# Performance work log

Hardware: AMD Instinct MI355X
Metric: run time of the kernel (lower is better)

Reference implementation:

```python
import jax, jax.numpy as jnp
import numpy as np
from jax import lax

N = 1024          # n_ligand == n_receptor == feature dim (required by broadcast in source)
D = 1024          # gnn_input_dim == gnn_output_dim
H = 32            # hopi_output_dim
C = 32            # cnn_channels


def setup_inputs() -> dict:
    key = jax.random.key(0)
    ks = jax.random.split(key, 24)
    s = 0.02
    inp = {
        "ligand_node_features": jax.random.normal(ks[0], (N, D), jnp.float32),
        "ligand_edge_features": jax.random.normal(ks[1], (N, D), jnp.float32),
        "ligand_adjacency": jax.random.uniform(ks[2], (N, N), jnp.float32),
        "receptor_node_features": jax.random.normal(ks[3], (N, D), jnp.float32),
        "receptor_edge_features": jax.random.normal(ks[4], (N, D), jnp.float32),
        "receptor_adjacency": jax.random.uniform(ks[5], (N, N), jnp.float32),
        # GNNLayer params (shared between ligand and receptor, as in source)
        "Wn": jax.random.normal(ks[6], (D, D), jnp.float32) * s,
        "bn": jax.random.normal(ks[7], (D,), jnp.float32) * s,
        "We": jax.random.normal(ks[8], (D, D), jnp.float32) * s,
        "be": jax.random.normal(ks[9], (D,), jnp.float32) * s,
        "Wa": jax.random.normal(ks[10], (1, D), jnp.float32) * s,
        "ba": jax.random.normal(ks[11], (1,), jnp.float32) * s,
        # HighOrderPairwiseInteraction: Linear(2*D -> H)
        "W_hopi": jax.random.normal(ks[12], (H, 2 * D), jnp.float32) * s,
        "b_hopi": jax.random.normal(ks[13], (H,), jnp.float32) * s,
        # CNN tail
        "conv1_w": jax.random.normal(ks[14], (C, H, 3, 3), jnp.float32) * s,
        "conv1_b": jax.random.normal(ks[15], (C,), jnp.float32) * s,
        "conv2_w": jax.random.normal(ks[16], (C, C, 3, 3), jnp.float32) * s,
        "conv2_b": jax.random.normal(ks[17], (C,), jnp.float32) * s,
        "conv3_w": jax.random.normal(ks[18], (1, C, 1, 1), jnp.float32) * s,
        "conv3_b": jax.random.normal(ks[19], (1,), jnp.float32) * s,
    }
    return inp


def _gnn(nf, ef, Wn, bn, We, be, Wa, ba):
    # aggregated: [N, D]
    agg = jnp.tanh(nf @ Wn.T + bn + ef @ We.T + be)
    scores = agg @ Wa.T + ba                      # [N, 1]
    attn = jax.nn.softmax(scores, axis=1)         # softmax over size-1 dim -> ones (faithful)
    weighted = jnp.sum(agg * attn, axis=1)        # [N]
    return nf + weighted                          # [N,D] + [N] broadcasts over last dim (D == N)


def _conv(x, w, b):
    y = lax.conv_general_dilated(x, w, (1, 1), "SAME",
                                 dimension_numbers=("NCHW", "OIHW", "NCHW"))
    return y + b[None, :, None, None]


def reference(ligand_node_features, ligand_edge_features, ligand_adjacency,
              receptor_node_features, receptor_edge_features, receptor_adjacency,
              Wn, bn, We, be, Wa, ba, W_hopi, b_hopi,
              conv1_w, conv1_b, conv2_w, conv2_b, conv3_w, conv3_b):
    lig = _gnn(ligand_node_features, ligand_edge_features, Wn, bn, We, be, Wa, ba)
    rec = _gnn(receptor_node_features, receptor_edge_features, Wn, bn, We, be, Wa, ba)

    # HOPI: interactions[i, j] = Linear(cat(lig[i], rec[j])) == lig[i] @ Wl.T + rec[j] @ Wr.T + b
    Wl, Wr = W_hopi[:, :D], W_hopi[:, D:]
    lig_p = lig @ Wl.T                            # [N, H]
    rec_p = rec @ Wr.T                            # [N, H]
    interactions = lig_p[:, None, :] + rec_p[None, :, :] + b_hopi  # [N, N, H]

    x = jnp.transpose(interactions, (2, 0, 1))[None]  # [1, H, N, N]
    x = jax.nn.relu(_conv(x, conv1_w, conv1_b))
    x = jax.nn.relu(_conv(x, conv2_w, conv2_b))
    x = _conv(x, conv3_w, conv3_b)                # [1, 1, N, N]
    return x[0, 0]                                # [N, N]
```

## Files before the change

### kernel.cpp

```cpp
#include <hip/hip_runtime.h>


typedef _Float16 half8 __attribute__((ext_vector_type(8)));
typedef _Float16 half4 __attribute__((ext_vector_type(4)));
typedef float    f32x4 __attribute__((ext_vector_type(4)));

__device__ __forceinline__ short f2h_bits(float f){
    _Float16 h = (_Float16)f;
    return __builtin_bit_cast(short, h);
}
__device__ __forceinline__ half8 pack2(const float4& x, const float4& y){
    half8 r;
    r[0] = (_Float16)x.x; r[1] = (_Float16)x.y;
    r[2] = (_Float16)x.z; r[3] = (_Float16)x.w;
    r[4] = (_Float16)y.x; r[5] = (_Float16)y.y;
    r[6] = (_Float16)y.z; r[7] = (_Float16)y.w;
    return r;
}
__device__ __forceinline__ half4 pack4(const float4& x){
    half4 r;
    r[0] = (_Float16)x.x; r[1] = (_Float16)x.y;
    r[2] = (_Float16)x.z; r[3] = (_Float16)x.w;
    return r;
}
__device__ __forceinline__ float tanh_fast(float x){
    float e = __expf(2.f * x);
    return 1.f - 2.f / (e + 1.f);
}

#define SWZ(c) ((((c) >> 1) & 3) << 3)

#define GNN_LOAD(AV, BV, KBN) {                                              \
    const int kbn_ = (KBN) & 2047;                                           \
    const float* Asrc_ = (kbn_ < 1024) ? A0 : A1;                            \
    const float* Bsrc_ = (kbn_ < 1024) ? Wn : We;                            \
    const int kk_ = kbn_ & 1023;                                             \
    const float* ap_ = Asrc_ + (size_t)(j0 + arow) * 1024 + kk_ + akc;       \
    const float* bp_ = Bsrc_ + (size_t)(d0 + brow) * 1024 + kk_ + bkc;       \
    AV[0] = *reinterpret_cast<const float4*>(ap_);                           \
    AV[1] = *reinterpret_cast<const float4*>(ap_ + 4);                       \
    AV[2] = *reinterpret_cast<const float4*>(ap_ + 8);                       \
    AV[3] = *reinterpret_cast<const float4*>(ap_ + 12);                      \
    BV[0] = *reinterpret_cast<const float4*>(bp_);                           \
    BV[1] = *reinterpret_cast<const float4*>(bp_ + 4);                       \
}

#define GNN_STAGE(AV, BV) {                                                  \
    const int ga_ = (t & 3) * 2;                                             \
    const int sa_ = arow & 7;                                                \
    *reinterpret_cast<half8*>(&As[arow * 64 + ((ga_    ) ^ sa_) * 8]) = pack2(AV[0], AV[1]); \
    *reinterpret_cast<half8*>(&As[arow * 64 + ((ga_ + 1) ^ sa_) * 8]) = pack2(AV[2], AV[3]); \
    *reinterpret_cast<half8*>(&Bs[brow * 64 + ((t & 7) ^ (brow & 7)) * 8]) = pack2(BV[0], BV[1]); \
}

#define GNN_MFMA() {                                                         \
    _Pragma("unroll")                                                        \
    for (int ks = 0; ks < 2; ++ks){                                          \
        half8 Af[2], Bf[2];                                                  \
        _Pragma("unroll")                                                    \
        for (int m = 0; m < 2; ++m){                                         \
            int row = wm * 32 + m * 16 + lr;                                 \
            int g   = ((ks * 4 + lg) ^ (row & 7)) * 8;                       \
            Af[m] = *reinterpret_cast<const half8*>(&As[row * 64 + g]);      \
        }                                                                    \
        _Pragma("unroll")                                                    \
        for (int n = 0; n < 2; ++n){                                         \
            int col = wn * 32 + n * 16 + lr;                                 \
            int g   = ((ks * 4 + lg) ^ (col & 7)) * 8;                       \
            Bf[n] = *reinterpret_cast<const half8*>(&Bs[col * 64 + g]);      \
        }                                                                    \
        _Pragma("unroll")                                                    \
        for (int m = 0; m < 2; ++m)                                          \
            _Pragma("unroll")                                                \
            for (int n = 0; n < 2; ++n)                                      \
                acc[m][n] = __builtin_amdgcn_mfma_f32_16x16x32_f16(          \
                    Af[m], Bf[n], acc[m][n], 0, 0, 0);                       \
    }                                                                        \
}

__global__ __launch_bounds__(512) void gnn_kernel(
    const float* __restrict__ lig_nf, const float* __restrict__ lig_ef,
    const float* __restrict__ rec_nf, const float* __restrict__ rec_ef,
    const float* __restrict__ Wn, const float* __restrict__ We,
    const float* __restrict__ bn, const float* __restrict__ be,
    float* __restrict__ part)
{
    __shared__ __attribute__((aligned(16))) short As[128 * 64];
    __shared__ __attribute__((aligned(16))) short Bs[64 * 64];
    __shared__ float red[128][2];

    const int t  = threadIdx.x;
    const int cx = blockIdx.z;
    const float* A0 = cx ? rec_nf : lig_nf;
    const float* A1 = cx ? rec_ef : lig_ef;
    const int j0 = blockIdx.x * 128;
    const int d0 = blockIdx.y * 64;

    const int wid  = t >> 6;
    const int wm   = wid >> 1;
    const int wn   = wid & 1;
    const int lane = t & 63;
    const int lr   = lane & 15;
    const int lg   = lane >> 4;

    f32x4 acc[2][2];
    #pragma unroll
    for (int m = 0; m < 2; ++m)
        #pragma unroll
        for (int n = 0; n < 2; ++n)
            acc[m][n] = (f32x4){0.f, 0.f, 0.f, 0.f};

    const int arow = t >> 2;
    const int akc  = (t & 3) * 16;
    const int brow = t >> 3;
    const int bkc  = (t & 7) * 8;

    float4 avA[4], bvA[2], avB[4], bvB[2];
    GNN_LOAD(avA, bvA, 0);
    GNN_LOAD(avB, bvB, 64);

    for (int kb = 0; kb < 2048; kb += 128){
        __syncthreads();
        GNN_STAGE(avA, bvA);
        GNN_LOAD(avA, bvA, kb + 128);
        __syncthreads();
        GNN_MFMA();
        __syncthreads();
        GNN_STAGE(avB, bvB);
        GNN_LOAD(avB, bvB, kb + 192);
        __syncthreads();
        GNN_MFMA();
    }

    float rowsum[2][4];
    #pragma unroll
    for (int m = 0; m < 2; ++m)
        #pragma unroll
        for (int jj = 0; jj < 4; ++jj) rowsum[m][jj] = 0.f;
    #pragma unroll
    for (int n = 0; n < 2; ++n){
        int d = d0 + wn * 32 + n * 16 + lr;
        float bias = bn[d] + be[d];
        #pragma unroll
        for (int m = 0; m < 2; ++m)
            #pragma unroll
            for (int jj = 0; jj < 4; ++jj)
                rowsum[m][jj] += tanh_fast(acc[m][n][jj] + bias);
    }
    #pragma unroll
    for (int mask = 1; mask < 16; mask <<= 1)
        #pragma unroll
        for (int m = 0; m < 2; ++m)
            #pragma unroll
            for (int jj = 0; jj < 4; ++jj)
                rowsum[m][jj] += __shfl_xor(rowsum[m][jj], mask);
    __syncthreads();
    if (lr == 0){
        #pragma unroll
        for (int m = 0; m < 2; ++m)
            #pragma unroll
            for (int jj = 0; jj < 4; ++jj)
                red[wm * 32 + m * 16 + lg * 4 + jj][wn] = rowsum[m][jj];
    }
    __syncthreads();
    if (t < 128)
        part[(size_t)cx * 16384 + (size_t)blockIdx.y * 1024 + j0 + t]
            = red[t][0] + red[t][1];
}

#define PP_LOAD(AV, BV, KBN) {                                               \
    const int kcol_ = (KBN) & 1023;                                          \
    _Pragma("unroll")                                                        \
    for (int p = 0; p < 3; ++p){                                             \
        int e_ = t + 512 * p;                                                \
        if (e_ < 1280){                                                      \
            int rowl_ = e_ >> 4;                                             \
            int grow_ = r0 - 8 + rowl_;                                      \
            if ((unsigned)grow_ < 1024u)                                     \
                AV[p] = *reinterpret_cast<const float4*>(                    \
                    nf + (size_t)grow_ * 1024 + kcol_ + (e_ & 15) * 4);      \
            else                                                             \
                AV[p] = make_float4(0.f, 0.f, 0.f, 0.f);                     \
        }                                                                    \
    }                                                                        \
    BV = *reinterpret_cast<const float4*>(                                   \
        W + (size_t)(t >> 4) * 2048 + kcol_ + (t & 15) * 4);                 \
}

#define PP_STAGE(AV, BV) {                                                   \
    _Pragma("unroll")                                                        \
    for (int p = 0; p < 3; ++p){                                             \
        int e_ = t + 512 * p;                                                \
        if (e_ < 1280){                                                      \
            int rowl_ = e_ >> 4;                                             \
            int ga_ = (e_ & 15) >> 1;                                        \
            int sub_ = (e_ & 1) * 4;                                         \
            *reinterpret_cast<half4*>(                                       \
                &As[rowl_ * 64 + ((ga_ ^ (rowl_ & 7)) * 8) + sub_]) = pack4(AV[p]); \
        }                                                                    \
    }                                                                        \
    {                                                                        \
        int row_ = t >> 4;                                                   \
        int ga_ = (t & 15) >> 1;                                             \
        int sub_ = (t & 1) * 4;                                              \
        *reinterpret_cast<half4*>(                                           \
            &Bs[row_ * 64 + ((ga_ ^ (row_ & 7)) * 8) + sub_]) = pack4(BV);   \
    }                                                                        \
}

#define PP_MFMA() {                                                          \
    if (wid < 5){                                                            \
        _Pragma("unroll")                                                    \
        for (int ks = 0; ks < 2; ++ks){                                      \
            int ar_ = wid * 16 + lr;                                         \
            half8 Af = *reinterpret_cast<const half8*>(                      \
                &As[ar_ * 64 + ((ks * 4 + lg) ^ (ar_ & 7)) * 8]);            \
            _Pragma("unroll")                                                \
            for (int n = 0; n < 2; ++n){                                     \
                int col_ = n * 16 + lr;                                      \
                half8 Bf = *reinterpret_cast<const half8*>(                  \
                    &Bs[col_ * 64 + ((ks * 4 + lg) ^ (col_ & 7)) * 8]);      \
                pacc[n] = __builtin_amdgcn_mfma_f32_16x16x32_f16(            \
                    Af, Bf, pacc[n], 0, 0, 0);                               \
            }                                                                \
        }                                                                    \
    }                                                                        \
}

__global__ __launch_bounds__(512) void pp_kernel(
    const float* __restrict__ lig_nf, const float* __restrict__ rec_nf,
    const float* __restrict__ W_hopi, const float* __restrict__ b_hopi,
    const float* __restrict__ w1, const float* __restrict__ b1,
    const float* __restrict__ w2,
    const float* __restrict__ part,
    float* __restrict__ Kp, short* __restrict__ U16, short* __restrict__ V16,
    short* __restrict__ w2f16)
{
    __shared__ __attribute__((aligned(16))) char smem[47232];
    const int t = threadIdx.x;
    const int role = blockIdx.x;

    if (role < 32){
        short* As = reinterpret_cast<short*>(smem);
        short* Bs = reinterpret_cast<short*>(smem + 10240);
        short* Pz = reinterpret_cast<short*>(smem + 14336);
        short* Ws = reinterpret_cast<short*>(smem + 20736);

        const int cx = role >> 4;
        const int r0 = (role & 15) * 64;
        const float* nf = cx ? rec_nf : lig_nf;
        const float* W  = W_hopi + (cx ? 1024 : 0);
        short* O = cx ? V16 : U16;

        const int wid = t >> 6;
        const int lane = t & 63;
        const int lr = lane & 15;
        const int lg = lane >> 4;

        f32x4 pacc[2];
        pacc[0] = (f32x4){0.f, 0.f, 0.f, 0.f};
        pacc[1] = (f32x4){0.f, 0.f, 0.f, 0.f};

        float4 avA[3], avB[3];
        float4 bvA, bvB;
        PP_LOAD(avA, bvA, 0);
        PP_LOAD(avB, bvB, 64);

        for (int kb = 0; kb < 1024; kb += 128){
            __syncthreads();
            PP_STAGE(avA, bvA);
            PP_LOAD(avA, bvA, kb + 128);
            __syncthreads();
            PP_MFMA();
            __syncthreads();
            PP_STAGE(avB, bvB);
            PP_LOAD(avB, bvB, kb + 192);
            __syncthreads();
            PP_MFMA();
        }

        if (wid < 5){
            #pragma unroll
            for (int n = 0; n < 2; ++n)
                #pragma unroll
                for (int jj = 0; jj < 4; ++jj){
                    int rowl = wid * 16 + lg * 4 + jj;
                    Pz[rowl * 40 + n * 16 + lr] = f2h_bits(pacc[n][jj]);
                }
        }

        #pragma unroll
        for (int q = 0; q < 2; ++q){
            int pr = t * 2 + q;
            int co = pr >> 5;
            int ci = pr & 31;
            const float* wp = w1 + co * 288 + ci * 9;
            float tap[9];
            #pragma unroll
            for (int e = 0; e < 9; ++e) tap[e] = wp[e];
            #pragma unroll
            for (int d = 0; d < 3; ++d){
                float ta, tb, tc;
                if (cx == 0){ ta = tap[d * 3 + 0]; tb = tap[d * 3 + 1]; tc = tap[d * 3 + 2]; }
                else        { ta = tap[0 + d];     tb = tap[3 + d];     tc = tap[6 + d]; }
                Ws[(0 * 32 + co) * 104 + d * 32 + ci] = f2h_bits(ta + tb + tc);
                Ws[(1 * 32 + co) * 104 + d * 32 + ci] = f2h_bits(tb + tc);
                Ws[(2 * 32 + co) * 104 + d * 32 + ci] = f2h_bits(ta + tb);
            }
        }
        __syncthreads();

        if (wid < 4){
            f32x4 uacc[3][2];
            #pragma unroll
            for (int cs = 0; cs < 3; ++cs)
                #pragma unroll
                for (int n = 0; n < 2; ++n)
                    uacc[cs][n] = (f32x4){0.f, 0.f, 0.f, 0.f};
            #pragma unroll
            for (int d = 0; d < 3; ++d){
                int ar = wid * 16 + lr;
                half8 Ap = *reinterpret_cast<const half8*>(
                    &Pz[(7 + ar + d) * 40 + lg * 8]);
                #pragma unroll
                for (int cs = 0; cs < 3; ++cs)
                    #pragma unroll
                    for (int n = 0; n < 2; ++n){
                        half8 Bp = *reinterpret_cast<const half8*>(
                            &Ws[(cs * 32 + n * 16 + lr) * 104 + d * 32 + lg * 8]);
                        uacc[cs][n] = __builtin_amdgcn_mfma_f32_16x16x32_f16(
                            Ap, Bp, uacc[cs][n], 0, 0, 0);
                    }
            }
            #pragma unroll
            for (int cs = 0; cs < 3; ++cs)
                #pragma unroll
                for (int n = 0; n < 2; ++n)
                    #pragma unroll
                    for (int jj = 0; jj < 4; ++jj){
                        int grow = r0 + wid * 16 + lg * 4 + jj;
                        O[((size_t)(cs << 10) + grow) * 32 + n * 16 + lr]
                            = f2h_bits(uacc[cs][n][jj]);
                    }
        }
        return;
    }

    if (role == 33){
        #pragma unroll
        for (int q = 0; q < 18; ++q){
            int e = t + q * 512;
            int co  = e / 288;
            int rem = e - co * 288;
            int ci  = rem / 9;
            int tap = rem - ci * 9;
            w2f16[(tap * 32 + co) * 32 + (ci ^ SWZ(co))] = f2h_bits(w2[e]);
        }
        return;
    }

    float* ws_l = reinterpret_cast<float*>(smem);
    float* ws_r = reinterpret_cast<float*>(smem + 4096);
    float* red  = reinterpret_cast<float*>(smem + 8192);
    float* cvs  = reinterpret_cast<float*>(smem + 10240);
    float* w1s  = reinterpret_cast<float*>(smem + 10368);

    #pragma unroll
    for (int q = 0; q < 5; ++q){
        int i4 = t + q * 512;
        if (i4 < 2304)
            *reinterpret_cast<float4*>(&w1s[i4 * 4]) =
                *reinterpret_cast<const float4*>(w1 + i4 * 4);
    }
    for (int j = t; j < 1024; j += 512){
        float sl = 0.f, sr = 0.f;
        #pragma unroll
        for (int b = 0; b < 16; ++b){
            sl += part[b * 1024 + j];
            sr += part[16384 + b * 1024 + j];
        }
        ws_l[j] = sl; ws_r[j] = sr;
    }
    __syncthreads();
    {
        const int h = t & 31;
        const int seg = t >> 5;
        const float* wl = W_hopi + (size_t)h * 2048 + seg * 64;
        const float* wr = wl + 1024;
        float s = 0.f;
        #pragma unroll 8
        for (int j = 0; j < 64; j += 4){
            float4 a = *reinterpret_cast<const float4*>(wl + j);
            float4 b = *reinterpret_cast<const float4*>(wr + j);
            const float* l = &ws_l[seg * 64 + j];
            const float* r = &ws_r[seg * 64 + j];
            s = fmaf(l[0], a.x, s); s = fmaf(l[1], a.y, s);
            s = fmaf(l[2], a.z, s); s = fmaf(l[3], a.w, s);
            s = fmaf(r[0], b.x, s); s = fmaf(r[1], b.y, s);
            s = fmaf(r[2], b.z, s); s = fmaf(r[3], b.w, s);
        }
        red[t] = s;
    }
    __syncthreads();
    if (t < 32){
        float tot = b_hopi[t];
        #pragma unroll
        for (int g = 0; g < 16; ++g) tot += red[g * 32 + t];
        cvs[t] = tot;
    }
    __syncthreads();
    for (int e = t; e < 288; e += 512){
        int co  = e & 31;
        int cse = e >> 5;
        int yc  = cse / 3, xc = cse - yc * 3;
        float sum = b1[co];
        for (int ci = 0; ci < 32; ++ci){
            const float* wp = &w1s[co * 288 + ci * 9];
            float t00 = wp[0], t01 = wp[1], t02 = wp[2];
            float t10 = wp[3], t11 = wp[4], t12 = wp[5];
            float t20 = wp[6], t21 = wp[7], t22 = wp[8];
            float r0, r1, r2;
            if (xc == 0){ r0 = t00+t01+t02; r1 = t10+t11+t12; r2 = t20+t21+t22; }
            else if (xc == 1){ r0 = t01+t02; r1 = t11+t12; r2 = t21+t22; }
            else { r0 = t00+t01; r1 = t10+t11; r2 = t20+t21; }
            float wsum = (yc == 0) ? (r0+r1+r2) : ((yc == 1) ? (r1+r2) : (r0+r1));
            sum = fmaf(cvs[ci], wsum, sum);
        }
        Kp[cse * 32 + co] = sum;
    }
}

__global__ __launch_bounds__(512) void conv_kernel(
    const short* __restrict__ U16, const short* __restrict__ V16,
    const float* __restrict__ Kp, const short* __restrict__ w2f16,
    const float* __restrict__ b2,
    const float* __restrict__ w3, const float* __restrict__ b3,
    float* __restrict__ outp)
{
    __shared__ __attribute__((aligned(16))) short ys[18 * 18 * 32];
    __shared__ __attribute__((aligned(16))) short wB[9 * 32 * 32];

    const int t    = threadIdx.x;
    const int oy0  = blockIdx.y * 16;
    const int ox0  = blockIdx.x * 16;
    const int wid  = t >> 6;
    const int lane = t & 63;
    const int lr   = lane & 15;
    const int lg   = lane >> 4;

    {
        const uint4* src = reinterpret_cast<const uint4*>(w2f16);
        uint4* dst = reinterpret_cast<uint4*>(wB);
        #pragma unroll
        for (int e = t; e < 1152; e += 512)
            dst[e] = src[e];
    }
    const bool interior = (blockIdx.x >= 1) & (blockIdx.x <= 62) &
                          (blockIdx.y >= 1) & (blockIdx.y <= 62);
    if (interior){
        const int cp = (t & 7) * 4;
        half4 k00;
        {
            float4 kf = *reinterpret_cast<const float4*>(&Kp[cp]);
            k00[0] = (_Float16)kf.x; k00[1] = (_Float16)kf.y;
            k00[2] = (_Float16)kf.z; k00[3] = (_Float16)kf.w;
        }
        #pragma unroll
        for (int pass = 0; pass < 6; ++pass){
            int idx = t + pass * 512;
            if (idx < 2592){
                int po  = idx >> 3;
                int ryo = po / 18;
                int rxo = po - ryo * 18;
                int gy = oy0 - 1 + ryo, gx = ox0 - 1 + rxo;
                half4 u = *reinterpret_cast<const half4*>(&U16[gy * 32 + cp]);
                half4 v = *reinterpret_cast<const half4*>(&V16[gx * 32 + cp]);
                half4 r = u + v + k00;
                #pragma unroll
                for (int e = 0; e < 4; ++e)
                    r[e] = r[e] > (_Float16)0.f ? r[e] : (_Float16)0.f;
                *reinterpret_cast<half4*>(&ys[po * 32 + (cp ^ SWZ(rxo))]) = r;
            }
        }
    } else {
        #pragma unroll
        for (int pass = 0; pass < 6; ++pass){
            int idx = t + pass * 512;
            if (idx < 2592){
                int po  = idx >> 3;
                int cp  = (idx & 7) * 4;
                int ryo = po / 18;
                int rxo = po - ryo * 18;
                int gy = oy0 - 1 + ryo, gx = ox0 - 1 + rxo;
                half4 h = {(_Float16)0.f, (_Float16)0.f, (_Float16)0.f, (_Float16)0.f};
                if ((unsigned)gy < 1024u && (unsigned)gx < 1024u){
                    int yc = (gy == 0) ? 1 : ((gy == 1023) ? 2 : 0);
                    int xc = (gx == 0) ? 1 : ((gx == 1023) ? 2 : 0);
                    half4 u = *reinterpret_cast<const half4*>(
                        &U16[((size_t)(xc << 10) + gy) * 32 + cp]);
                    half4 v = *reinterpret_cast<const half4*>(
                        &V16[((size_t)(yc << 10) + gx) * 32 + cp]);
                    float4 k = *reinterpret_cast<const float4*>(&Kp[(yc * 3 + xc) * 32 + cp]);
                    h[0] = (_Float16)fmaxf((float)u[0] + (float)v[0] + k.x, 0.f);
                    h[1] = (_Float16)fmaxf((float)u[1] + (float)v[1] + k.y, 0.f);
                    h[2] = (_Float16)fmaxf((float)u[2] + (float)v[2] + k.z, 0.f);
                    h[3] = (_Float16)fmaxf((float)u[3] + (float)v[3] + k.w, 0.f);
                }
                *reinterpret_cast<half4*>(&ys[po * 32 + (cp ^ SWZ(rxo))]) = h;
            }
        }
    }
    __syncthreads();

    {
        half8 Bf[2][9];
        float bias[2], w3v[2];
        #pragma unroll
        for (int n = 0; n < 2; ++n){
            int co = n * 16 + lr;
            bias[n] = b2[co];
            w3v[n]  = w3[co];
            #pragma unroll
            for (int tap = 0; tap < 9; ++tap)
                Bf[n][tap] = *reinterpret_cast<const half8*>(
                    &wB[(tap * 32 + co) * 32 + ((lg * 8) ^ SWZ(co))]);
        }
        const float b3v = b3[0];
        for (int s = wid; s < 16; s += 8){
            int p  = s * 16 + lr;
            int ry = p >> 4;
            int rx = p & 15;
            f32x4 acc0 = {0.f, 0.f, 0.f, 0.f};
            f32x4 acc1 = {0.f, 0.f, 0.f, 0.f};
            #pragma unroll
            for (int tap = 0; tap < 9; ++tap){
                const int dy = tap / 3, dx = tap - (tap / 3) * 3;
                int pix = (ry + dy) * 18 + rx + dx;
                half8 A = *reinterpret_cast<const half8*>(
                    &ys[pix * 32 + ((lg * 8) ^ SWZ(rx + dx))]);
                acc0 = __builtin_amdgcn_mfma_f32_16x16x32_f16(A, Bf[0][tap], acc0, 0, 0, 0);
                acc1 = __builtin_amdgcn_mfma_f32_16x16x32_f16(A, Bf[1][tap], acc1, 0, 0, 0);
            }
            float part[4];
            #pragma unroll
            for (int j = 0; j < 4; ++j)
                part[j] = w3v[0] * fmaxf(acc0[j] + bias[0], 0.f)
                        + w3v[1] * fmaxf(acc1[j] + bias[1], 0.f);
            #pragma unroll
            for (int m = 1; m < 16; m <<= 1)
                #pragma unroll
                for (int j = 0; j < 4; ++j)
                    part[j] += __shfl_xor(part[j], m);
            if (lr == 0){
                float4 o = make_float4(part[0] + b3v, part[1] + b3v,
                                       part[2] + b3v, part[3] + b3v);
                *reinterpret_cast<float4*>(outp + (size_t)(oy0 + s) * 1024 + ox0 + lg * 4) = o;
            }
        }
    }
}

extern "C" void kernel_launch(void* const* d_in, const int* in_sizes, int n_in,
                              void* d_out, int out_size, void* d_ws, size_t ws_size,
                              hipStream_t stream)
{
    const float* lig_nf = (const float*)d_in[0];
    const float* lig_ef = (const float*)d_in[1];
    const float* rec_nf = (const float*)d_in[3];
    const float* rec_ef = (const float*)d_in[4];
    const float* Wn     = (const float*)d_in[6];
    const float* bn     = (const float*)d_in[7];
    const float* We     = (const float*)d_in[8];
    const float* be     = (const float*)d_in[9];
    const float* W_hopi = (const float*)d_in[12];
    const float* b_hopi = (const float*)d_in[13];
    const float* w1     = (const float*)d_in[14];
    const float* b1     = (const float*)d_in[15];
    const float* w2     = (const float*)d_in[16];
    const float* b2     = (const float*)d_in[17];
    const float* w3     = (const float*)d_in[18];
    const float* b3     = (const float*)d_in[19];
    float* outp = (float*)d_out;

    float* part  = (float*)d_ws;
    float* Kp    = (float*)((char*)d_ws + 393216);
    short* U16   = (short*)((char*)d_ws + 394368);
    short* V16   = (short*)((char*)d_ws + 590976);
    short* w2f16 = (short*)((char*)d_ws + 787584);

    dim3 g1(8, 16, 2);
    gnn_kernel<<<g1, 512, 0, stream>>>(lig_nf, lig_ef, rec_nf, rec_ef,
                                       Wn, We, bn, be, part);
    pp_kernel<<<34, 512, 0, stream>>>(lig_nf, rec_nf, W_hopi, b_hopi,
                                      w1, b1, w2, part, Kp, U16, V16, w2f16);
    dim3 g3(64, 64);
    conv_kernel<<<g3, 512, 0, stream>>>(U16, V16, Kp, w2f16, b2, w3, b3, outp);
}
```

Baseline: 114.0 us.

## Build conv2 A-fragments in registers instead of staging relu tile in LDS

Removes the 18x18x32 shared-memory staging of the conv1 output (relu(U+V+K)) and instead has each lane compute its MFMA A operand directly from U16/V16 rows held in registers, reusing three U and three V vectors across the nine taps. This drops the shared-memory write, the barrier and the swizzled LDS reads, and lowers LDS use, which may raise occupancy. In exchange each halo value is recomputed per tap (extra VALU adds and relus), and the border path issues more global loads per tap.

```diff
diff --git a/kernel.cpp b/kernel.cpp
--- a/kernel.cpp
+++ b/kernel.cpp
@@ -437,7 +437,6 @@
     const float* __restrict__ w3, const float* __restrict__ b3,
     float* __restrict__ outp)
 {
-    __shared__ __attribute__((aligned(16))) short ys[18 * 18 * 32];
     __shared__ __attribute__((aligned(16))) short wB[9 * 32 * 32];
 
     const int t    = threadIdx.x;
@@ -447,6 +446,7 @@
     const int lane = t & 63;
     const int lr   = lane & 15;
     const int lg   = lane >> 4;
+    const int c8   = lg * 8;
 
     {
         const uint4* src = reinterpret_cast<const uint4*>(w2f16);
@@ -455,107 +455,97 @@
         for (int e = t; e < 1152; e += 512)
             dst[e] = src[e];
     }
+    __syncthreads();
+
+    half8 Bf[2][9];
+    float bias[2], w3v[2];
+    #pragma unroll
+    for (int n = 0; n < 2; ++n){
+        int co = n * 16 + lr;
+        bias[n] = b2[co];
+        w3v[n]  = w3[co];
+        #pragma unroll
+        for (int tap = 0; tap < 9; ++tap)
+            Bf[n][tap] = *reinterpret_cast<const half8*>(
+                &wB[(tap * 32 + co) * 32 + ((lg * 8) ^ SWZ(co))]);
+    }
+    const float b3v = b3[0];
+
     const bool interior = (blockIdx.x >= 1) & (blockIdx.x <= 62) &
                           (blockIdx.y >= 1) & (blockIdx.y <= 62);
+
+    half8 k00;
     if (interior){
-        const int cp = (t & 7) * 4;
-        half4 k00;
-        {
-            float4 kf = *reinterpret_cast<const float4*>(&Kp[cp]);
-            k00[0] = (_Float16)kf.x; k00[1] = (_Float16)kf.y;
-            k00[2] = (_Float16)kf.z; k00[3] = (_Float16)kf.w;
-        }
-        #pragma unroll
-        for (int pass = 0; pass < 6; ++pass){
-            int idx = t + pass * 512;
-            if (idx < 2592){
-                int po  = idx >> 3;
-                int ryo = po / 18;
-                int rxo = po - ryo * 18;
-                int gy = oy0 - 1 + ryo, gx = ox0 - 1 + rxo;
-                half4 u = *reinterpret_cast<const half4*>(&U16[gy * 32 + cp]);
-                half4 v = *reinterpret_cast<const half4*>(&V16[gx * 32 + cp]);
-                half4 r = u + v + k00;
+        float4 ka = *reinterpret_cast<const float4*>(&Kp[c8]);
+        float4 kb = *reinterpret_cast<const float4*>(&Kp[c8 + 4]);
+        k00 = pack2(ka, kb);
+    }
+
+    #pragma unroll
+    for (int si = 0; si < 2; ++si){
+        const int s  = wid + si * 8;
+        f32x4 acc0 = {0.f, 0.f, 0.f, 0.f};
+        f32x4 acc1 = {0.f, 0.f, 0.f, 0.f};
+
+        if (interior){
+            const int gyb = oy0 - 1 + s;
+            const int gxb = ox0 - 1 + lr;
+            half8 uk[3], vv[3];
+            #pragma unroll
+            for (int d = 0; d < 3; ++d){
+                uk[d] = *reinterpret_cast<const half8*>(&U16[(gyb + d) * 32 + c8]) + k00;
+                vv[d] = *reinterpret_cast<const half8*>(&V16[(gxb + d) * 32 + c8]);
+            }
+            #pragma unroll
+            for (int tap = 0; tap < 9; ++tap){
+                const int dy = tap / 3, dx = tap - (tap / 3) * 3;
+                half8 A = uk[dy] + vv[dx];
                 #pragma unroll
-                for (int e = 0; e < 4; ++e)
-                    r[e] = r[e] > (_Float16)0.f ? r[e] : (_Float16)0.f;
-                *reinterpret_cast<half4*>(&ys[po * 32 + (cp ^ SWZ(rxo))]) = r;
+                for (int e = 0; e < 8; ++e)
+                    A[e] = A[e] > (_Float16)0.f ? A[e] : (_Float16)0.f;
+                acc0 = __builtin_amdgcn_mfma_f32_16x16x32_f16(A, Bf[0][tap], acc0, 0, 0, 0);
+                acc1 = __builtin_amdgcn_mfma_f32_16x16x32_f16(A, Bf[1][tap], acc1, 0, 0, 0);
             }
-        }
-    } else {
-        #pragma unroll
-        for (int pass = 0; pass < 6; ++pass){
-            int idx = t + pass * 512;
-            if (idx < 2592){
-                int po  = idx >> 3;
-                int cp  = (idx & 7) * 4;
-                int ryo = po / 18;
-                int rxo = po - ryo * 18;
-                int gy = oy0 - 1 + ryo, gx = ox0 - 1 + rxo;
-                half4 h = {(_Float16)0.f, (_Float16)0.f, (_Float16)0.f, (_Float16)0.f};
+        } else {
+            #pragma unroll
+            for (int tap = 0; tap < 9; ++tap){
+                const int dy = tap / 3, dx = tap - (tap / 3) * 3;
+                int gy = oy0 - 1 + s + dy;
+                int gx = ox0 - 1 + lr + dx;
+                half8 A;
+                #pragma unroll
+                for (int e = 0; e < 8; ++e) A[e] = (_Float16)0.f;
                 if ((unsigned)gy < 1024u && (unsigned)gx < 1024u){
                     int yc = (gy == 0) ? 1 : ((gy == 1023) ? 2 : 0);
                     int xc = (gx == 0) ? 1 : ((gx == 1023) ? 2 : 0);
-                    half4 u = *reinterpret_cast<const half4*>(
-                        &U16[((size_t)(xc << 10) + gy) * 32 + cp]);
-                    half4 v = *reinterpret_cast<const half4*>(
-                        &V16[((size_t)(yc << 10) + gx) * 32 + cp]);
-                    float4 k = *reinterpret_cast<const float4*>(&Kp[(yc * 3 + xc) * 32 + cp]);
-                    h[0] = (_Float16)fmaxf((float)u[0] + (float)v[0] + k.x, 0.f);
-                    h[1] = (_Float16)fmaxf((float)u[1] + (float)v[1] + k.y, 0.f);
-                    h[2] = (_Float16)fmaxf((float)u[2] + (float)v[2] + k.z, 0.f);
-                    h[3] = (_Float16)fmaxf((float)u[3] + (float)v[3] + k.w, 0.f);
+                    half8 u = *reinterpret_cast<const half8*>(
+                        &U16[((size_t)(xc << 10) + gy) * 32 + c8]);
+                    half8 v = *reinterpret_cast<const half8*>(
+                        &V16[((size_t)(yc << 10) + gx) * 32 + c8]);
+                    const float* kp = &Kp[(yc * 3 + xc) * 32 + c8];
+                    #pragma unroll
+                    for (int e = 0; e < 8; ++e)
+                        A[e] = (_Float16)fmaxf((float)u[e] + (float)v[e] + kp[e], 0.f);
                 }
-                *reinterpret_cast<half4*>(&ys[po * 32 + (cp ^ SWZ(rxo))]) = h;
-            }
-        }
-    }
-    __syncthreads();
-
-    {
-        half8 Bf[2][9];
-        float bias[2], w3v[2];
-        #pragma unroll
-        for (int n = 0; n < 2; ++n){
-            int co = n * 16 + lr;
-            bias[n] = b2[co];
-            w3v[n]  = w3[co];
-            #pragma unroll
-            for (int tap = 0; tap < 9; ++tap)
-                Bf[n][tap] = *reinterpret_cast<const half8*>(
-                    &wB[(tap * 32 + co) * 32 + ((lg * 8) ^ SWZ(co))]);
-        }
-        const float b3v = b3[0];
-        for (int s = wid; s < 16; s += 8){
-            int p  = s * 16 + lr;
-            int ry = p >> 4;
-            int rx = p & 15;
-            f32x4 acc0 = {0.f, 0.f, 0.f, 0.f};
-            f32x4 acc1 = {0.f, 0.f, 0.f, 0.f};
-            #pragma unroll
-            for (int tap = 0; tap < 9; ++tap){
-                const int dy = tap / 3, dx = tap - (tap / 3) * 3;
-                int pix = (ry + dy) * 18 + rx + dx;
-                half8 A = *reinterpret_cast<const half8*>(
-                    &ys[pix * 32 + ((lg * 8) ^ SWZ(rx + dx))]);
                 acc0 = __builtin_amdgcn_mfma_f32_16x16x32_f16(A, Bf[0][tap], acc0, 0, 0, 0);
                 acc1 = __builtin_amdgcn_mfma_f32_16x16x32_f16(A, Bf[1][tap], acc1, 0, 0, 0);
             }
-            float part[4];
+        }
+
+        float part[4];
+        #pragma unroll
+        for (int j = 0; j < 4; ++j)
+            part[j] = w3v[0] * fmaxf(acc0[j] + bias[0], 0.f)
+                    + w3v[1] * fmaxf(acc1[j] + bias[1], 0.f);
+        #pragma unroll
+        for (int m = 1; m < 16; m <<= 1)
             #pragma unroll
             for (int j = 0; j < 4; ++j)
-                part[j] = w3v[0] * fmaxf(acc0[j] + bias[0], 0.f)
-                        + w3v[1] * fmaxf(acc1[j] + bias[1], 0.f);
-            #pragma unroll
-            for (int m = 1; m < 16; m <<= 1)
-                #pragma unroll
-                for (int j = 0; j < 4; ++j)
-                    part[j] += __shfl_xor(part[j], m);
-            if (lr == 0){
-                float4 o = make_float4(part[0] + b3v, part[1] + b3v,
-                                       part[2] + b3v, part[3] + b3v);
-                *reinterpret_cast<float4*>(outp + (size_t)(oy0 + s) * 1024 + ox0 + lg * 4) = o;
-            }
+                part[j] += __shfl_xor(part[j], m);
+        if (lr == 0){
+            float4 o = make_float4(part[0] + b3v, part[1] + b3v,
+                                   part[2] + b3v, part[3] + b3v);
+            *reinterpret_cast<float4*>(outp + (size_t)(oy0 + s) * 1024 + ox0 + lg * 4) = o;
         }
     }
 }
```

New measurement: 145.8 us. +28.0%, slower.

## Load MFMA operands directly from global memory, dropping LDS staging in pp_kernel

Applied to the files above, without the earlier changes.

Replaces the double-buffered LDS-staged GEMM in the projection part of pp_kernel with a loop where each of the five active waves loads its A and B fragments straight from global memory into registers and issues MFMAs. This removes the four __syncthreads per iteration and the LDS write/read traffic. In exchange, global loads are less coalesced (strided rows with 32-byte chunks per lane), W rows are re-read by every wave, and only 5 of 8 waves take part in loading.

```diff
diff --git a/kernel.cpp b/kernel.cpp
--- a/kernel.cpp
+++ b/kernel.cpp
@@ -168,65 +168,6 @@
             = red[t][0] + red[t][1];
 }
 
-#define PP_LOAD(AV, BV, KBN) {                                               \
-    const int kcol_ = (KBN) & 1023;                                          \
-    _Pragma("unroll")                                                        \
-    for (int p = 0; p < 3; ++p){                                             \
-        int e_ = t + 512 * p;                                                \
-        if (e_ < 1280){                                                      \
-            int rowl_ = e_ >> 4;                                             \
-            int grow_ = r0 - 8 + rowl_;                                      \
-            if ((unsigned)grow_ < 1024u)                                     \
-                AV[p] = *reinterpret_cast<const float4*>(                    \
-                    nf + (size_t)grow_ * 1024 + kcol_ + (e_ & 15) * 4);      \
-            else                                                             \
-                AV[p] = make_float4(0.f, 0.f, 0.f, 0.f);                     \
-        }                                                                    \
-    }                                                                        \
-    BV = *reinterpret_cast<const float4*>(                                   \
-        W + (size_t)(t >> 4) * 2048 + kcol_ + (t & 15) * 4);                 \
-}
-
-#define PP_STAGE(AV, BV) {                                                   \
-    _Pragma("unroll")                                                        \
-    for (int p = 0; p < 3; ++p){                                             \
-        int e_ = t + 512 * p;                                                \
-        if (e_ < 1280){                                                      \
-            int rowl_ = e_ >> 4;                                             \
-            int ga_ = (e_ & 15) >> 1;                                        \
-            int sub_ = (e_ & 1) * 4;                                         \
-            *reinterpret_cast<half4*>(                                       \
-                &As[rowl_ * 64 + ((ga_ ^ (rowl_ & 7)) * 8) + sub_]) = pack4(AV[p]); \
-        }                                                                    \
-    }                                                                        \
-    {                                                                        \
-        int row_ = t >> 4;                                                   \
-        int ga_ = (t & 15) >> 1;                                             \
-        int sub_ = (t & 1) * 4;                                              \
-        *reinterpret_cast<half4*>(                                           \
-            &Bs[row_ * 64 + ((ga_ ^ (row_ & 7)) * 8) + sub_]) = pack4(BV);   \
-    }                                                                        \
-}
-
-#define PP_MFMA() {                                                          \
-    if (wid < 5){                                                            \
-        _Pragma("unroll")                                                    \
-        for (int ks = 0; ks < 2; ++ks){                                      \
-            int ar_ = wid * 16 + lr;                                         \
-            half8 Af = *reinterpret_cast<const half8*>(                      \
-                &As[ar_ * 64 + ((ks * 4 + lg) ^ (ar_ & 7)) * 8]);            \
-            _Pragma("unroll")                                                \
-            for (int n = 0; n < 2; ++n){                                     \
-                int col_ = n * 16 + lr;                                      \
-                half8 Bf = *reinterpret_cast<const half8*>(                  \
-                    &Bs[col_ * 64 + ((ks * 4 + lg) ^ (col_ & 7)) * 8]);      \
-                pacc[n] = __builtin_amdgcn_mfma_f32_16x16x32_f16(            \
-                    Af, Bf, pacc[n], 0, 0, 0);                               \
-            }                                                                \
-        }                                                                    \
-    }                                                                        \
-}
-
 __global__ __launch_bounds__(512) void pp_kernel(
     const float* __restrict__ lig_nf, const float* __restrict__ rec_nf,
     const float* __restrict__ W_hopi, const float* __restrict__ b_hopi,
@@ -241,8 +182,6 @@
     const int role = blockIdx.x;
 
     if (role < 32){
-        short* As = reinterpret_cast<short*>(smem);
-        short* Bs = reinterpret_cast<short*>(smem + 10240);
         short* Pz = reinterpret_cast<short*>(smem + 14336);
         short* Ws = reinterpret_cast<short*>(smem + 20736);
 
@@ -261,25 +200,30 @@
         pacc[0] = (f32x4){0.f, 0.f, 0.f, 0.f};
         pacc[1] = (f32x4){0.f, 0.f, 0.f, 0.f};
 
-        float4 avA[3], avB[3];
-        float4 bvA, bvB;
-        PP_LOAD(avA, bvA, 0);
-        PP_LOAD(avB, bvB, 64);
-
-        for (int kb = 0; kb < 1024; kb += 128){
-            __syncthreads();
-            PP_STAGE(avA, bvA);
-            PP_LOAD(avA, bvA, kb + 128);
-            __syncthreads();
-            PP_MFMA();
-            __syncthreads();
-            PP_STAGE(avB, bvB);
-            PP_LOAD(avB, bvB, kb + 192);
-            __syncthreads();
-            PP_MFMA();
-        }
-
         if (wid < 5){
+            const int lrow = wid * 16 + lr;
+            const int grow = r0 - 8 + lrow;
+            const bool ok = (unsigned)grow < 1024u;
+            const float* ap = nf + (size_t)(ok ? grow : 0) * 1024 + lg * 8;
+            const float* b0 = W + (size_t)lr * 2048 + lg * 8;
+            const float* b1p = W + (size_t)(16 + lr) * 2048 + lg * 8;
+
+            #pragma unroll 4
+            for (int kb = 0; kb < 1024; kb += 32){
+                float4 a0 = make_float4(0.f, 0.f, 0.f, 0.f);
+                float4 a1 = a0;
+                if (ok){
+                    a0 = *reinterpret_cast<const float4*>(ap + kb);
+                    a1 = *reinterpret_cast<const float4*>(ap + kb + 4);
+                }
+                half8 Af = pack2(a0, a1);
+                half8 B0 = pack2(*reinterpret_cast<const float4*>(b0 + kb),
+                                 *reinterpret_cast<const float4*>(b0 + kb + 4));
+                half8 B1 = pack2(*reinterpret_cast<const float4*>(b1p + kb),
+                                 *reinterpret_cast<const float4*>(b1p + kb + 4));
+                pacc[0] = __builtin_amdgcn_mfma_f32_16x16x32_f16(Af, B0, pacc[0], 0, 0, 0);
+                pacc[1] = __builtin_amdgcn_mfma_f32_16x16x32_f16(Af, B1, pacc[1], 0, 0, 0);
+            }
             #pragma unroll
             for (int n = 0; n < 2; ++n)
                 #pragma unroll
```

After: 114.2 us. Within noise of the previous version (+0.2%).
